# Performance work log

Measured on AMD Instinct MI355X. Metric: run time of the kernel, lower is better.

## Reference

```python
import jax, jax.numpy as jnp
import numpy as np

N, E, G = 100_000, 1_200_000, 256
EPS = 1e-5

def _bn(a, g, b):
    # BatchNorm1d in training mode: biased batch statistics over dim 0
    mu = a.mean(0)
    var = ((a - mu) ** 2).mean(0)
    return (a - mu) * jax.lax.rsqrt(var + EPS) * g + b

def _cgconv(x, src, dst, ea, Wf, bf, Ws, bs, g, b):
    # PyG CGConv: z = [x_i, x_j, edge_attr]; m = sigmoid(lin_f(z)) * softplus(lin_s(z));
    # out = BN(scatter_add(m -> dst)) + x
    z = jnp.concatenate([x[dst], x[src], ea], axis=-1)      # [E, 2*64+1]
    m = jax.nn.sigmoid(z @ Wf + bf) * jax.nn.softplus(z @ Ws + bs)  # [E, 64]
    agg = jax.ops.segment_sum(m, dst, num_segments=x.shape[0])
    return _bn(agg, g, b) + x

def setup_inputs() -> dict:
    key = jax.random.key(0)
    ks = jax.random.split(key, 16)
    def w(k, shape, scale):
        return jax.random.normal(k, shape, jnp.float32) * scale
    inp = {
        "x": jax.random.normal(ks[0], (N, 12), jnp.float32),
        "edge_index": jax.random.randint(ks[1], (2, E), 0, N, jnp.int32),
        "edge_attr": jax.random.uniform(ks[2], (E, 1), dtype=jnp.float32),
        "batch": jnp.sort(jax.random.randint(ks[3], (N,), 0, G, jnp.int32)),
        "W_in": w(ks[4], (12, 64), 0.3), "b_in": jnp.zeros((64,), jnp.float32),
        "g0": jnp.ones((64,), jnp.float32), "beta0": jnp.zeros((64,), jnp.float32),
    }
    i = 5
    for l in (1, 2, 3):
        inp[f"Wf{l}"] = w(ks[i], (129, 64), 0.1)
        inp[f"bf{l}"] = jnp.zeros((64,), jnp.float32)
        inp[f"Ws{l}"] = w(ks[i + 1], (129, 64), 0.1)
        inp[f"bs{l}"] = jnp.zeros((64,), jnp.float32)
        inp[f"g{l}"] = jnp.ones((64,), jnp.float32)
        inp[f"bb{l}"] = jnp.zeros((64,), jnp.float32)
        i += 2
    inp["W1"] = w(ks[11], (64, 32), 0.15)
    inp["b1"] = jnp.zeros((32,), jnp.float32)
    inp["W2"] = w(ks[12], (32, 1), 0.2)
    inp["b2"] = jnp.zeros((1,), jnp.float32)
    return inp

def reference(x, edge_index, edge_attr, batch,
              W_in, b_in, g0, beta0,
              Wf1, bf1, Ws1, bs1, g1, bb1,
              Wf2, bf2, Ws2, bs2, g2, bb2,
              Wf3, bf3, Ws3, bs3, g3, bb3,
              W1, b1, W2, b2):
    src, dst = edge_index[0], edge_index[1]
    h = jax.nn.relu(_bn(x @ W_in + b_in, g0, beta0))
    h = jax.nn.relu(_cgconv(h, src, dst, edge_attr, Wf1, bf1, Ws1, bs1, g1, bb1))
    h = jax.nn.relu(_cgconv(h, src, dst, edge_attr, Wf2, bf2, Ws2, bs2, g2, bb2))
    h = _cgconv(h, src, dst, edge_attr, Wf3, bf3, Ws3, bs3, g3, bb3)
    # global_mean_pool
    s = jax.ops.segment_sum(h, batch, num_segments=G)
    c = jax.ops.segment_sum(jnp.ones((h.shape[0],), h.dtype), batch, num_segments=G)
    pooled = s / jnp.maximum(c, 1.0)[:, None]
    return jax.nn.relu(pooled @ W1 + b1) @ W2 + b2  # [G, 1]
```

## Files before the change

### kernel.cpp

```cpp
#include <hip/hip_runtime.h>
#include <math.h>

#define N_NODES 100000
#define N_EDGES 1200000
#define N_GRAPHS 256
#define CH 64
#define NC (N_NODES * CH)
#define EPS 1e-5f
#define LOG2E 1.4426950408889634f
#define LN2 0.6931471805599453f
#define EA_SCALE 32768.0f

#define SCAN_NB 98
#define ZSTRN 72
#define GTILES ((N_NODES + 63) / 64)
#define EA_BLOCKS 4096
#define NW (EA_BLOCKS * 4)
#define POOL_BLOCKS 256

#define NCOLORS 8
#define SC_BLOCKS 2048
#define NCHUNK (SC_BLOCKS / NCOLORS)
#define CSZ ((N_EDGES + NCHUNK - 1) / NCHUNK)
#define RNODES ((N_NODES + NCOLORS - 1) / NCOLORS)

typedef _Float16 half8 __attribute__((ext_vector_type(8)));
typedef _Float16 half2v __attribute__((ext_vector_type(2)));
typedef float floatx4 __attribute__((ext_vector_type(4)));

__device__ __forceinline__ int lbound(const int* __restrict__ a, int n, int v) {
    int lo = 0, hi = n;
    while (lo < hi) {
        int mid = (lo + hi) >> 1;
        if (a[mid] < v) lo = mid + 1; else hi = mid;
    }
    return lo;
}

__device__ __forceinline__ float gate2(float f2, float s2) {
    float ef = __builtin_amdgcn_exp2f(-f2);
    float sig = __builtin_amdgcn_rcpf(1.0f + ef);
    float es = __builtin_amdgcn_exp2f(-fabsf(s2));
    float sp = fmaxf(s2, 0.0f) + __builtin_amdgcn_logf(1.0f + es);
    return sig * sp;
}

__global__ void embed_stats_kernel(const float* __restrict__ x,
                                   const float* __restrict__ W,
                                   const float* __restrict__ b,
                                   float* __restrict__ out,
                                   float* __restrict__ stats) {
    int c = threadIdx.x & 63;
    int sub = threadIdx.x >> 6;
    float s = 0.f, q = 0.f;
    for (int r = blockIdx.x * 4 + sub; r < N_NODES; r += gridDim.x * 4) {
        const float* xr = x + r * 12;
        float acc = b[c];
#pragma unroll
        for (int k = 0; k < 12; ++k)
            acc = fmaf(xr[k], W[k * CH + c], acc);
        out[(size_t)r * CH + c] = acc;
        s += acc;
        q = fmaf(acc, acc, q);
    }
    __shared__ float ls[4][64];
    __shared__ float lq[4][64];
    ls[sub][c] = s;
    lq[sub][c] = q;
    __syncthreads();
    if (sub == 0) {
        s = ls[0][c] + ls[1][c] + ls[2][c] + ls[3][c];
        q = lq[0][c] + lq[1][c] + lq[2][c] + lq[3][c];
        atomicAdd(&stats[c], s);
        atomicAdd(&stats[64 + c], q);
    }
}

__global__ void hist_kernel(const int* __restrict__ ei,
                            int* __restrict__ rowptr) {
    const int j = blockIdx.x & (NCOLORS - 1);
    const int k = blockIdx.x >> 3;
    const int dlo = j * RNODES;
    const int dhi = min(N_NODES, dlo + RNODES);
    const int e0 = k * CSZ;
    const int e1 = min(N_EDGES, e0 + CSZ);
    for (int e = e0 + threadIdx.x; e < e1; e += 256) {
        int d = ei[N_EDGES + e];
        if (d >= dlo && d < dhi) atomicAdd(&rowptr[d + 1], 1);
    }
}

__global__ void scanA_kernel(int* __restrict__ a, int* __restrict__ btot) {
    __shared__ int wsum[16];
    int t = threadIdx.x, lane = t & 63, w = t >> 6;
    int i = blockIdx.x * 1024 + t;
    int v = (i <= N_NODES) ? a[i] : 0;
    int s = v;
#pragma unroll
    for (int d = 1; d < 64; d <<= 1) {
        int o = __shfl_up(s, d);
        if (lane >= d) s += o;
    }
    if (lane == 63) wsum[w] = s;
    __syncthreads();
    if (w == 0) {
        int ws2 = (lane < 16) ? wsum[lane] : 0;
#pragma unroll
        for (int d = 1; d < 16; d <<= 1) {
            int o = __shfl_up(ws2, d);
            if (lane >= d) ws2 += o;
        }
        if (lane < 16) wsum[lane] = ws2;
    }
    __syncthreads();
    int off = (w > 0) ? wsum[w - 1] : 0;
    if (i <= N_NODES) a[i] = s + off;
    if (t == 0) btot[blockIdx.x] = wsum[15];
}

__global__ void scanB_kernel(int* __restrict__ btot) {
    int lane = threadIdx.x;
    int carry = 0;
    for (int base = 0; base < SCAN_NB; base += 64) {
        int i = base + lane;
        int v = (i < SCAN_NB) ? btot[i] : 0;
        int s = v;
#pragma unroll
        for (int d = 1; d < 64; d <<= 1) {
            int o = __shfl_up(s, d);
            if (lane >= d) s += o;
        }
        if (i < SCAN_NB) btot[i] = s + carry;
        carry += __shfl(s, 63);
    }
}

__global__ void scanC_kernel(int* __restrict__ a, const int* __restrict__ btot,
                             int* __restrict__ cursor) {
    int i = blockIdx.x * 1024 + threadIdx.x;
    int off = (blockIdx.x > 0) ? btot[blockIdx.x - 1] : 0;
    if (i <= N_NODES) {
        int val = a[i] + off;
        a[i] = val;
        if (i < N_NODES) cursor[i] = val;
    }
}

__global__ void scatter_kernel(const int* __restrict__ ei,
                               const float* __restrict__ ea,
                               int* __restrict__ cursor,
                               unsigned* __restrict__ sef,
                               const int* __restrict__ rowptr,
                               int* __restrict__ wrange) {
    int gid = blockIdx.x * blockDim.x + threadIdx.x;
    if (gid <= NW) {
        if (gid == NW) wrange[NW] = N_NODES;
        else {
            int e0t = (int)((long)gid * N_EDGES / NW);
            wrange[gid] = lbound(rowptr, N_NODES + 1, e0t);
        }
    }
    const int j = blockIdx.x & (NCOLORS - 1);
    const int k = blockIdx.x >> 3;
    const int dlo = j * RNODES;
    const int dhi = min(N_NODES, dlo + RNODES);
    const int e0 = k * CSZ;
    const int e1 = min(N_EDGES, e0 + CSZ);
    for (int e = e0 + threadIdx.x; e < e1; e += 256) {
        int d = ei[N_EDGES + e];
        if (d >= dlo && d < dhi) {
            int pos = atomicAdd(&cursor[d], 1);
            unsigned v = ((unsigned)ei[e] << 15) | (unsigned)(ea[e] * EA_SCALE);
            sef[pos] = v;
        }
    }
}

__global__ void prep_weights_kernel(const float* __restrict__ Wf0, const float* __restrict__ Ws0,
                                    const float* __restrict__ bf0, const float* __restrict__ bs0,
                                    const float* __restrict__ Wf1, const float* __restrict__ Ws1,
                                    const float* __restrict__ bf1, const float* __restrict__ bs1,
                                    const float* __restrict__ Wf2, const float* __restrict__ Ws2,
                                    const float* __restrict__ bf2, const float* __restrict__ bs2,
                                    _Float16* __restrict__ WT2,
                                    float* __restrict__ w128,
                                    float* __restrict__ bias) {
    int gid = blockIdx.x * blockDim.x + threadIdx.x;
    int l = gid >> 14;
    int idx = gid & 16383;
    if (l >= 3) return;
    const float* Wf = (l == 0) ? Wf0 : (l == 1) ? Wf1 : Wf2;
    const float* Ws = (l == 0) ? Ws0 : (l == 1) ? Ws1 : Ws2;
    const float* bf = (l == 0) ? bf0 : (l == 1) ? bf1 : bf2;
    const float* bs = (l == 0) ? bs0 : (l == 1) ? bs1 : bs2;
    {
        int cc = idx >> 6;
        int k = idx & 63;
        float v;
        if (cc < 128) {
            int ch = cc >> 1;
            v = (cc & 1) ? Ws[k * 64 + ch] : Wf[k * 64 + ch];
        } else {
            int j = cc - 128, ch = j >> 1;
            v = (j & 1) ? Ws[(64 + k) * 64 + ch] : Wf[(64 + k) * 64 + ch];
        }
        WT2[l * 16384 + idx] = (_Float16)(v * LOG2E);
    }
    if (idx < 128) {
        w128[l * 128 + idx] = ((idx < 64) ? Wf[128 * 64 + idx] : Ws[128 * 64 + (idx - 64)])
                              * (LOG2E / EA_SCALE);
        bias[l * 128 + idx] = ((idx < 64) ? bf[idx] : bs[idx - 64]) * LOG2E;
    }
}

template <bool RES>
__global__ __launch_bounds__(256)
void node_gemm_kernel(const float* __restrict__ ain,
                      const float* __restrict__ res,
                      const float* __restrict__ stats,
                      const float* __restrict__ gamma,
                      const float* __restrict__ beta,
                      const _Float16* __restrict__ WT2,
                      float* __restrict__ hout,
                      _Float16* __restrict__ pqrs) {
    __shared__ __align__(16) _Float16 As[64 * ZSTRN];
    __shared__ __align__(16) float ab[128];
    const int t = threadIdx.x;
    const int lane = t & 63;
    const int w = t >> 6;
    const int l15 = lane & 15;
    const int quad = lane >> 4;

    if (t < 64) {
        float mean = stats[t] * (1.0f / (float)N_NODES);
        float var  = stats[64 + t] * (1.0f / (float)N_NODES) - mean * mean;
        float inv  = rsqrtf(var + EPS);
        float A = gamma[t] * inv;
        ab[t] = A;
        ab[64 + t] = beta[t] - mean * A;
    }

    half8 bfr[4][2];
#pragma unroll
    for (int tt = 0; tt < 4; ++tt)
#pragma unroll
        for (int ks = 0; ks < 2; ++ks)
            bfr[tt][ks] = *(const half8*)(WT2 + (w * 64 + tt * 16 + l15) * 64 + ks * 32 + quad * 8);
    __syncthreads();

    const int base = blockIdx.x * 64;
    {
        const int e = t >> 2, q = t & 3;
        const int row = base + e;
        const bool valid = (row < N_NODES);
        const int crow = valid ? row : (N_NODES - 1);
        const float* ap = ain + (size_t)crow * CH + q * 16;
        const float* rp = res + (size_t)crow * CH + q * 16;
        float vv[16];
#pragma unroll
        for (int i = 0; i < 4; ++i) {
            float4 a4 = *(const float4*)(ap + i * 4);
            float4 A4 = *(const float4*)(ab + q * 16 + i * 4);
            float4 B4 = *(const float4*)(ab + 64 + q * 16 + i * 4);
            float rx = 0.f, ry = 0.f, rz = 0.f, rw = 0.f;
            if (RES) {
                float4 r4 = *(const float4*)(rp + i * 4);
                rx = r4.x; ry = r4.y; rz = r4.z; rw = r4.w;
            }
            vv[i * 4 + 0] = fmaxf(fmaf(a4.x, A4.x, B4.x) + rx, 0.0f);
            vv[i * 4 + 1] = fmaxf(fmaf(a4.y, A4.y, B4.y) + ry, 0.0f);
            vv[i * 4 + 2] = fmaxf(fmaf(a4.z, A4.z, B4.z) + rz, 0.0f);
            vv[i * 4 + 3] = fmaxf(fmaf(a4.w, A4.w, B4.w) + rw, 0.0f);
        }
        if (valid) {
            float* hp = hout + (size_t)row * CH + q * 16;
#pragma unroll
            for (int i = 0; i < 4; ++i)
                *(float4*)(hp + i * 4) = make_float4(vv[i * 4], vv[i * 4 + 1], vv[i * 4 + 2], vv[i * 4 + 3]);
        }
        half8 o;
#pragma unroll
        for (int j = 0; j < 8; ++j) o[j] = (_Float16)vv[j];
        *(half8*)(As + e * ZSTRN + q * 16) = o;
#pragma unroll
        for (int j = 0; j < 8; ++j) o[j] = (_Float16)vv[8 + j];
        *(half8*)(As + e * ZSTRN + q * 16 + 8) = o;
    }
    __syncthreads();

    floatx4 acc[4][4];
#pragma unroll
    for (int rt = 0; rt < 4; ++rt)
#pragma unroll
        for (int tt = 0; tt < 4; ++tt)
#pragma unroll
            for (int r = 0; r < 4; ++r) acc[rt][tt][r] = 0.f;

#pragma unroll
    for (int ks = 0; ks < 2; ++ks) {
#pragma unroll
        for (int rt = 0; rt < 4; ++rt) {
            half8 a = *(const half8*)(As + (rt * 16 + l15) * ZSTRN + ks * 32 + quad * 8);
#pragma unroll
            for (int tt = 0; tt < 4; ++tt)
                acc[rt][tt] = __builtin_amdgcn_mfma_f32_16x16x32_f16(a, bfr[tt][ks], acc[rt][tt], 0, 0, 0);
        }
    }

#pragma unroll
    for (int rt = 0; rt < 4; ++rt) {
#pragma unroll
        for (int r = 0; r < 4; ++r) {
            int row = base + rt * 16 + quad * 4 + r;
            if (row < N_NODES) {
#pragma unroll
                for (int tt = 0; tt < 4; ++tt)
                    pqrs[(size_t)row * 256 + w * 64 + tt * 16 + l15] = (_Float16)acc[rt][tt][r];
            }
        }
    }
}

__global__ __launch_bounds__(256)
void edge_agg_kernel(const _Float16* __restrict__ pqrs,
                     const unsigned* __restrict__ sef,
                     const int* __restrict__ rowptr,
                     const int* __restrict__ wrange,
                     const float* __restrict__ w128,
                     const float* __restrict__ bias,
                     float* __restrict__ agg,
                     float* __restrict__ wpart) {
    const int lane = threadIdx.x & 63;
    const int w = threadIdx.x >> 6;
    const int gw = __builtin_amdgcn_readfirstlane(blockIdx.x * 4 + w);
    const float wfc = w128[lane], wsc = w128[64 + lane];
    const float bfc = bias[lane], bsc = bias[64 + lane];
    const half2v* __restrict__ prb = (const half2v*)pqrs;
    const half2v* __restrict__ qsb = (const half2v*)pqrs + 64;

    const int n0 = wrange[gw];
    const int n1 = wrange[gw + 1];

    float ssum = 0.f, sqsum = 0.f;
    for (int n = n0; n < n1; ++n) {
        const int rs = rowptr[n], re = rowptr[n + 1];
        half2v pr = prb[(size_t)n * 128 + lane];
        const float fb = (float)pr[0] + bfc;
        const float sb = (float)pr[1] + bsc;
        float acc0 = 0.f, acc1 = 0.f, acc2 = 0.f, acc3 = 0.f;
        int e = rs;
        for (; e + 8 <= re; e += 8) {
            unsigned s0 = sef[e],     s1 = sef[e + 1], s2 = sef[e + 2], s3 = sef[e + 3];
            unsigned s4 = sef[e + 4], s5 = sef[e + 5], s6 = sef[e + 6], s7 = sef[e + 7];
            half2v q0 = qsb[(size_t)(s0 >> 15) * 128 + lane];
            half2v q1 = qsb[(size_t)(s1 >> 15) * 128 + lane];
            half2v q2 = qsb[(size_t)(s2 >> 15) * 128 + lane];
            half2v q3 = qsb[(size_t)(s3 >> 15) * 128 + lane];
            half2v q4 = qsb[(size_t)(s4 >> 15) * 128 + lane];
            half2v q5 = qsb[(size_t)(s5 >> 15) * 128 + lane];
            half2v q6 = qsb[(size_t)(s6 >> 15) * 128 + lane];
            half2v q7 = qsb[(size_t)(s7 >> 15) * 128 + lane];
            float ea0 = (float)(s0 & 32767u), ea1 = (float)(s1 & 32767u);
            float ea2 = (float)(s2 & 32767u), ea3 = (float)(s3 & 32767u);
            float ea4 = (float)(s4 & 32767u), ea5 = (float)(s5 & 32767u);
            float ea6 = (float)(s6 & 32767u), ea7 = (float)(s7 & 32767u);
            acc0 += gate2(fmaf(ea0, wfc, fb + (float)q0[0]), fmaf(ea0, wsc, sb + (float)q0[1]));
            acc1 += gate2(fmaf(ea1, wfc, fb + (float)q1[0]), fmaf(ea1, wsc, sb + (float)q1[1]));
            acc2 += gate2(fmaf(ea2, wfc, fb + (float)q2[0]), fmaf(ea2, wsc, sb + (float)q2[1]));
            acc3 += gate2(fmaf(ea3, wfc, fb + (float)q3[0]), fmaf(ea3, wsc, sb + (float)q3[1]));
            acc0 += gate2(fmaf(ea4, wfc, fb + (float)q4[0]), fmaf(ea4, wsc, sb + (float)q4[1]));
            acc1 += gate2(fmaf(ea5, wfc, fb + (float)q5[0]), fmaf(ea5, wsc, sb + (float)q5[1]));
            acc2 += gate2(fmaf(ea6, wfc, fb + (float)q6[0]), fmaf(ea6, wsc, sb + (float)q6[1]));
            acc3 += gate2(fmaf(ea7, wfc, fb + (float)q7[0]), fmaf(ea7, wsc, sb + (float)q7[1]));
        }
        if (e + 4 <= re) {
            unsigned s0 = sef[e], s1 = sef[e + 1], s2 = sef[e + 2], s3 = sef[e + 3];
            half2v q0 = qsb[(size_t)(s0 >> 15) * 128 + lane];
            half2v q1 = qsb[(size_t)(s1 >> 15) * 128 + lane];
            half2v q2 = qsb[(size_t)(s2 >> 15) * 128 + lane];
            half2v q3 = qsb[(size_t)(s3 >> 15) * 128 + lane];
            float ea0 = (float)(s0 & 32767u), ea1 = (float)(s1 & 32767u);
            float ea2 = (float)(s2 & 32767u), ea3 = (float)(s3 & 32767u);
            acc0 += gate2(fmaf(ea0, wfc, fb + (float)q0[0]), fmaf(ea0, wsc, sb + (float)q0[1]));
            acc1 += gate2(fmaf(ea1, wfc, fb + (float)q1[0]), fmaf(ea1, wsc, sb + (float)q1[1]));
            acc2 += gate2(fmaf(ea2, wfc, fb + (float)q2[0]), fmaf(ea2, wsc, sb + (float)q2[1]));
            acc3 += gate2(fmaf(ea3, wfc, fb + (float)q3[0]), fmaf(ea3, wsc, sb + (float)q3[1]));
            e += 4;
        }
        for (; e < re; ++e) {
            unsigned s0 = sef[e];
            half2v q0 = qsb[(size_t)(s0 >> 15) * 128 + lane];
            float ea0 = (float)(s0 & 32767u);
            acc0 += gate2(fmaf(ea0, wfc, fb + (float)q0[0]), fmaf(ea0, wsc, sb + (float)q0[1]));
        }
        float acc = LN2 * ((acc0 + acc1) + (acc2 + acc3));
        agg[(size_t)n * CH + lane] = acc;
        ssum += acc;
        sqsum = fmaf(acc, acc, sqsum);
    }
    __shared__ float reds[4][128];
    reds[w][lane] = ssum;
    reds[w][64 + lane] = sqsum;
    __syncthreads();
    if (w == 0) {
        float a = reds[0][lane] + reds[1][lane] + reds[2][lane] + reds[3][lane];
        float b = reds[0][64 + lane] + reds[1][64 + lane] + reds[2][64 + lane] + reds[3][64 + lane];
        wpart[(size_t)blockIdx.x * 128 + lane] = a;
        wpart[(size_t)blockIdx.x * 128 + 64 + lane] = b;
    }
}

__global__ __launch_bounds__(256)
void reduce_stats_kernel(const float* __restrict__ wpart,
                         float* __restrict__ stats) {
    __shared__ float red[2][128];
    const int col = threadIdx.x & 127;
    const int rg = threadIdx.x >> 7;
    const int rows = EA_BLOCKS / 128;
    const int r0 = blockIdx.x * rows;
    float s = 0.f;
    for (int r = r0 + rg; r < r0 + rows; r += 2)
        s += wpart[(size_t)r * 128 + col];
    red[rg][col] = s;
    __syncthreads();
    if (rg == 0) atomicAdd(&stats[col], red[0][col] + red[1][col]);
}

__global__ __launch_bounds__(256)
void pool_bn_kernel(const float* __restrict__ ain,
                    const float* __restrict__ res,
                    const float* __restrict__ stats,
                    const float* __restrict__ gamma,
                    const float* __restrict__ beta,
                    const int* __restrict__ batch,
                    float* __restrict__ pooled,
                    float* __restrict__ counts) {
    __shared__ float ab[128];
    if (threadIdx.x < 64) {
        int t = threadIdx.x;
        float mean = stats[t] * (1.0f / (float)N_NODES);
        float var  = stats[64 + t] * (1.0f / (float)N_NODES) - mean * mean;
        float inv  = rsqrtf(var + EPS);
        float A = gamma[t] * inv;
        ab[t] = A;
        ab[64 + t] = beta[t] - mean * A;
    }
    __syncthreads();

    const int c = threadIdx.x & 63;
    const float A = ab[c], B = ab[64 + c];
    const int walker = blockIdx.x * 4 + (threadIdx.x >> 6);
    const int nwalk = POOL_BLOCKS * 4;
    const int chunk = (N_NODES + nwalk - 1) / nwalk;
    int r0 = walker * chunk;
    int r1 = min(N_NODES, r0 + chunk);
    if (r0 >= r1) return;

    int cur = batch[r0];
    float acc = 0.0f;
    int runlen = 0;
    for (int r = r0; r < r1; ++r) {
        int b = batch[r];
        if (b != cur) {
            atomicAdd(&pooled[cur * CH + c], acc);
            if (c == 0) atomicAdd(&counts[cur], (float)runlen);
            acc = 0.0f;
            runlen = 0;
            cur = b;
        }
        size_t idx = (size_t)r * CH + c;
        acc += fmaf(ain[idx], A, B) + res[idx];
        ++runlen;
    }
    atomicAdd(&pooled[cur * CH + c], acc);
    if (c == 0) atomicAdd(&counts[cur], (float)runlen);
}

__global__ void head_kernel(const float* __restrict__ pooled,
                            const float* __restrict__ counts,
                            const float* __restrict__ W1,
                            const float* __restrict__ b1,
                            const float* __restrict__ W2,
                            const float* __restrict__ b2,
                            float* __restrict__ out) {
    int gph = blockIdx.x;
    int t = threadIdx.x;
    __shared__ float p[64];
    __shared__ float h1[32];
    float cnt = fmaxf(counts[gph], 1.0f);
    p[t] = pooled[gph * CH + t] / cnt;
    __syncthreads();
    if (t < 32) {
        float acc = b1[t];
#pragma unroll
        for (int c = 0; c < 64; ++c)
            acc = fmaf(p[c], W1[c * 32 + t], acc);
        h1[t] = fmaxf(acc, 0.0f);
    }
    __syncthreads();
    if (t == 0) {
        float acc = b2[0];
#pragma unroll
        for (int j = 0; j < 32; ++j)
            acc = fmaf(h1[j], W2[j], acc);
        out[gph] = acc;
    }
}

extern "C" void kernel_launch(void* const* d_in, const int* in_sizes, int n_in,
                              void* d_out, int out_size, void* d_ws, size_t ws_size,
                              hipStream_t stream) {
    const float* x     = (const float*)d_in[0];
    const int*   ei    = (const int*)d_in[1];
    const float* ea    = (const float*)d_in[2];
    const int*   batch = (const int*)d_in[3];
    const float* W_in  = (const float*)d_in[4];
    const float* b_in  = (const float*)d_in[5];
    const float* g0    = (const float*)d_in[6];
    const float* beta0 = (const float*)d_in[7];

    const float* Wf[3] = {(const float*)d_in[8],  (const float*)d_in[14], (const float*)d_in[20]};
    const float* bfv[3]= {(const float*)d_in[9],  (const float*)d_in[15], (const float*)d_in[21]};
    const float* Wsv[3]= {(const float*)d_in[10], (const float*)d_in[16], (const float*)d_in[22]};
    const float* bsv[3]= {(const float*)d_in[11], (const float*)d_in[17], (const float*)d_in[23]};
    const float* gm[3] = {(const float*)d_in[12], (const float*)d_in[18], (const float*)d_in[24]};
    const float* bb[3] = {(const float*)d_in[13], (const float*)d_in[19], (const float*)d_in[25]};

    const float* W1 = (const float*)d_in[26];
    const float* b1 = (const float*)d_in[27];
    const float* W2 = (const float*)d_in[28];
    const float* b2 = (const float*)d_in[29];

    float* out = (float*)d_out;

    char* base = (char*)d_ws;
    size_t off = 0;
    float* bufA = (float*)(base + off);       off += (size_t)NC * 4;
    float* bufB = (float*)(base + off);       off += (size_t)NC * 4;
    float* AGG  = (float*)(base + off);       off += (size_t)NC * 4;
    _Float16* WT2 = (_Float16*)(base + off);  off += 3 * 256 * 64 * 2;
    float* w128   = (float*)(base + off);     off += 3 * 128 * 4;
    float* biasL  = (float*)(base + off);     off += 3 * 128 * 4;
    int* cursor   = (int*)(base + off);       off += (size_t)N_NODES * 4;
    unsigned* sef = (unsigned*)(base + off);  off += (size_t)N_EDGES * 4;
    _Float16* pqrs = (_Float16*)(base + off); off += (size_t)N_NODES * 256 * 2;
    float* wpart  = (float*)(base + off);     off += (size_t)EA_BLOCKS * 128 * 4;
    int* wrange   = (int*)(base + off);       off += (size_t)(NW + 1) * 4;
    char* zbase   = base + off;
    int* rowptr   = (int*)(base + off);       off += (size_t)(N_NODES + 1) * 4;
    int* btot     = (int*)(base + off);       off += SCAN_NB * 4;
    float* stats4 = (float*)(base + off);     off += 4 * 128 * 4;
    float* pooled = (float*)(base + off);     off += (size_t)N_GRAPHS * CH * 4;
    float* counts = (float*)(base + off);     off += (size_t)N_GRAPHS * 4;
    size_t zbytes = (size_t)(base + off - zbase);

    hipMemsetAsync(zbase, 0, zbytes, stream);

    hist_kernel<<<SC_BLOCKS, 256, 0, stream>>>(ei, rowptr);
    scanA_kernel<<<SCAN_NB, 1024, 0, stream>>>(rowptr, btot);
    scanB_kernel<<<1, 64, 0, stream>>>(btot);
    scanC_kernel<<<SCAN_NB, 1024, 0, stream>>>(rowptr, btot, cursor);
    scatter_kernel<<<SC_BLOCKS, 256, 0, stream>>>(ei, ea, cursor, sef, rowptr, wrange);

    prep_weights_kernel<<<192, 256, 0, stream>>>(
        Wf[0], Wsv[0], bfv[0], bsv[0],
        Wf[1], Wsv[1], bfv[1], bsv[1],
        Wf[2], Wsv[2], bfv[2], bsv[2],
        WT2, w128, biasL);

    embed_stats_kernel<<<512, 256, 0, stream>>>(x, W_in, b_in, bufA, stats4);

    node_gemm_kernel<false><<<GTILES, 256, 0, stream>>>(
        bufA, nullptr, stats4, g0, beta0, WT2 + 0 * 256 * 64, bufB, pqrs);
    edge_agg_kernel<<<EA_BLOCKS, 256, 0, stream>>>(
        pqrs, sef, rowptr, wrange, w128 + 0 * 128, biasL + 0 * 128, AGG, wpart);
    reduce_stats_kernel<<<128, 256, 0, stream>>>(wpart, stats4 + 128);

    node_gemm_kernel<true><<<GTILES, 256, 0, stream>>>(
        AGG, bufB, stats4 + 128, gm[0], bb[0], WT2 + 1 * 256 * 64, bufA, pqrs);
    edge_agg_kernel<<<EA_BLOCKS, 256, 0, stream>>>(
        pqrs, sef, rowptr, wrange, w128 + 1 * 128, biasL + 1 * 128, AGG, wpart);
    reduce_stats_kernel<<<128, 256, 0, stream>>>(wpart, stats4 + 256);

    node_gemm_kernel<true><<<GTILES, 256, 0, stream>>>(
        AGG, bufA, stats4 + 256, gm[1], bb[1], WT2 + 2 * 256 * 64, bufB, pqrs);
    edge_agg_kernel<<<EA_BLOCKS, 256, 0, stream>>>(
        pqrs, sef, rowptr, wrange, w128 + 2 * 128, biasL + 2 * 128, AGG, wpart);
    reduce_stats_kernel<<<128, 256, 0, stream>>>(wpart, stats4 + 384);

    pool_bn_kernel<<<POOL_BLOCKS, 256, 0, stream>>>(
        AGG, bufB, stats4 + 384, gm[2], bb[2], batch, pooled, counts);
    head_kernel<<<N_GRAPHS, 64, 0, stream>>>(pooled, counts, W1, b1, W2, b2, out);
}
```

Before: 605.6 us.

## Flatten edge loop across nodes with double-buffered software-pipelined gathers

Replaces the per-node edge loop in the aggregation kernel with one flat loop over each wave's whole edge range. It issues the next 8 index loads and feature gathers into a second register set while the current 8 are consumed, and flushes node results when a row boundary is crossed. This is meant to keep more gathers in flight and avoid short-row tails and per-node loop overhead. It adds data-dependent branches per edge, more registers for the two buffers, and pads the edge array by 8 entries to cover overreads.

```diff
diff --git a/kernel.cpp b/kernel.cpp
--- a/kernel.cpp
+++ b/kernel.cpp
@@ -160,6 +160,7 @@
             wrange[gid] = lbound(rowptr, N_NODES + 1, e0t);
         }
     }
+    if (gid < 8) sef[N_EDGES + gid] = 0u;
     const int j = blockIdx.x & (NCOLORS - 1);
     const int k = blockIdx.x >> 3;
     const int dlo = j * RNODES;
@@ -321,6 +322,56 @@
     }
 }
 
+#define EA_ISSUE(p, base) \
+    r##p##0 = sef[(base) + 0]; r##p##1 = sef[(base) + 1]; \
+    r##p##2 = sef[(base) + 2]; r##p##3 = sef[(base) + 3]; \
+    r##p##4 = sef[(base) + 4]; r##p##5 = sef[(base) + 5]; \
+    r##p##6 = sef[(base) + 6]; r##p##7 = sef[(base) + 7]; \
+    q##p##0 = qsb[(size_t)(r##p##0 >> 15) * 128 + lane]; \
+    q##p##1 = qsb[(size_t)(r##p##1 >> 15) * 128 + lane]; \
+    q##p##2 = qsb[(size_t)(r##p##2 >> 15) * 128 + lane]; \
+    q##p##3 = qsb[(size_t)(r##p##3 >> 15) * 128 + lane]; \
+    q##p##4 = qsb[(size_t)(r##p##4 >> 15) * 128 + lane]; \
+    q##p##5 = qsb[(size_t)(r##p##5 >> 15) * 128 + lane]; \
+    q##p##6 = qsb[(size_t)(r##p##6 >> 15) * 128 + lane]; \
+    q##p##7 = qsb[(size_t)(r##p##7 >> 15) * 128 + lane];
+
+#define EA_FLUSH(ei_) \
+    do { \
+        float av_ = LN2 * acc; \
+        agg[(size_t)n * CH + lane] = av_; \
+        ssum += av_; sqsum = fmaf(av_, av_, sqsum); \
+        acc = 0.f; \
+        ++n; \
+        prc = prn; \
+        { int np_ = (n + 1 < N_NODES) ? (n + 1) : (N_NODES - 1); \
+          prn = prb[(size_t)np_ * 128 + lane]; } \
+        re = rowptr[n + 1]; \
+    } while (re == (ei_)); \
+    fb = (float)prc[0] + bfc; \
+    sb2 = (float)prc[1] + bsc;
+
+#define EA_EDGE(ei_, rv_, qv_) { \
+    if ((ei_) == re) { EA_FLUSH(ei_); } \
+    float eaf_ = (float)((rv_) & 32767u); \
+    float f2_ = fmaf(eaf_, wfc, fb + (float)(qv_)[0]); \
+    float s2_ = fmaf(eaf_, wsc, sb2 + (float)(qv_)[1]); \
+    acc += gate2(f2_, s2_); }
+
+#define EA_EDGE_G(ei_, rv_, qv_) if ((ei_) < E1) EA_EDGE(ei_, rv_, qv_)
+
+#define EA_CONS8(p, base) \
+    EA_EDGE((base) + 0, r##p##0, q##p##0) EA_EDGE((base) + 1, r##p##1, q##p##1) \
+    EA_EDGE((base) + 2, r##p##2, q##p##2) EA_EDGE((base) + 3, r##p##3, q##p##3) \
+    EA_EDGE((base) + 4, r##p##4, q##p##4) EA_EDGE((base) + 5, r##p##5, q##p##5) \
+    EA_EDGE((base) + 6, r##p##6, q##p##6) EA_EDGE((base) + 7, r##p##7, q##p##7)
+
+#define EA_TAIL8(p, base) \
+    EA_EDGE_G((base) + 0, r##p##0, q##p##0) EA_EDGE_G((base) + 1, r##p##1, q##p##1) \
+    EA_EDGE_G((base) + 2, r##p##2, q##p##2) EA_EDGE_G((base) + 3, r##p##3, q##p##3) \
+    EA_EDGE_G((base) + 4, r##p##4, q##p##4) EA_EDGE_G((base) + 5, r##p##5, q##p##5) \
+    EA_EDGE_G((base) + 6, r##p##6, q##p##6) EA_EDGE_G((base) + 7, r##p##7, q##p##7)
+
 __global__ __launch_bounds__(256)
 void edge_agg_kernel(const _Float16* __restrict__ pqrs,
                      const unsigned* __restrict__ sef,
@@ -342,61 +393,50 @@
     const int n1 = wrange[gw + 1];
 
     float ssum = 0.f, sqsum = 0.f;
-    for (int n = n0; n < n1; ++n) {
-        const int rs = rowptr[n], re = rowptr[n + 1];
-        half2v pr = prb[(size_t)n * 128 + lane];
-        const float fb = (float)pr[0] + bfc;
-        const float sb = (float)pr[1] + bsc;
-        float acc0 = 0.f, acc1 = 0.f, acc2 = 0.f, acc3 = 0.f;
-        int e = rs;
-        for (; e + 8 <= re; e += 8) {
-            unsigned s0 = sef[e],     s1 = sef[e + 1], s2 = sef[e + 2], s3 = sef[e + 3];
-            unsigned s4 = sef[e + 4], s5 = sef[e + 5], s6 = sef[e + 6], s7 = sef[e + 7];
-            half2v q0 = qsb[(size_t)(s0 >> 15) * 128 + lane];
-            half2v q1 = qsb[(size_t)(s1 >> 15) * 128 + lane];
-            half2v q2 = qsb[(size_t)(s2 >> 15) * 128 + lane];
-            half2v q3 = qsb[(size_t)(s3 >> 15) * 128 + lane];
-            half2v q4 = qsb[(size_t)(s4 >> 15) * 128 + lane];
-            half2v q5 = qsb[(size_t)(s5 >> 15) * 128 + lane];
-            half2v q6 = qsb[(size_t)(s6 >> 15) * 128 + lane];
-            half2v q7 = qsb[(size_t)(s7 >> 15) * 128 + lane];
-            float ea0 = (float)(s0 & 32767u), ea1 = (float)(s1 & 32767u);
-            float ea2 = (float)(s2 & 32767u), ea3 = (float)(s3 & 32767u);
-            float ea4 = (float)(s4 & 32767u), ea5 = (float)(s5 & 32767u);
-            float ea6 = (float)(s6 & 32767u), ea7 = (float)(s7 & 32767u);
-            acc0 += gate2(fmaf(ea0, wfc, fb + (float)q0[0]), fmaf(ea0, wsc, sb + (float)q0[1]));
-            acc1 += gate2(fmaf(ea1, wfc, fb + (float)q1[0]), fmaf(ea1, wsc, sb + (float)q1[1]));
-            acc2 += gate2(fmaf(ea2, wfc, fb + (float)q2[0]), fmaf(ea2, wsc, sb + (float)q2[1]));
-            acc3 += gate2(fmaf(ea3, wfc, fb + (float)q3[0]), fmaf(ea3, wsc, sb + (float)q3[1]));
-            acc0 += gate2(fmaf(ea4, wfc, fb + (float)q4[0]), fmaf(ea4, wsc, sb + (float)q4[1]));
-            acc1 += gate2(fmaf(ea5, wfc, fb + (float)q5[0]), fmaf(ea5, wsc, sb + (float)q5[1]));
-            acc2 += gate2(fmaf(ea6, wfc, fb + (float)q6[0]), fmaf(ea6, wsc, sb + (float)q6[1]));
-            acc3 += gate2(fmaf(ea7, wfc, fb + (float)q7[0]), fmaf(ea7, wsc, sb + (float)q7[1]));
-        }
-        if (e + 4 <= re) {
-            unsigned s0 = sef[e], s1 = sef[e + 1], s2 = sef[e + 2], s3 = sef[e + 3];
-            half2v q0 = qsb[(size_t)(s0 >> 15) * 128 + lane];
-            half2v q1 = qsb[(size_t)(s1 >> 15) * 128 + lane];
-            half2v q2 = qsb[(size_t)(s2 >> 15) * 128 + lane];
-            half2v q3 = qsb[(size_t)(s3 >> 15) * 128 + lane];
-            float ea0 = (float)(s0 & 32767u), ea1 = (float)(s1 & 32767u);
-            float ea2 = (float)(s2 & 32767u), ea3 = (float)(s3 & 32767u);
-            acc0 += gate2(fmaf(ea0, wfc, fb + (float)q0[0]), fmaf(ea0, wsc, sb + (float)q0[1]));
-            acc1 += gate2(fmaf(ea1, wfc, fb + (float)q1[0]), fmaf(ea1, wsc, sb + (float)q1[1]));
-            acc2 += gate2(fmaf(ea2, wfc, fb + (float)q2[0]), fmaf(ea2, wsc, sb + (float)q2[1]));
-            acc3 += gate2(fmaf(ea3, wfc, fb + (float)q3[0]), fmaf(ea3, wsc, sb + (float)q3[1]));
-            e += 4;
-        }
-        for (; e < re; ++e) {
-            unsigned s0 = sef[e];
-            half2v q0 = qsb[(size_t)(s0 >> 15) * 128 + lane];
-            float ea0 = (float)(s0 & 32767u);
-            acc0 += gate2(fmaf(ea0, wfc, fb + (float)q0[0]), fmaf(ea0, wsc, sb + (float)q0[1]));
-        }
-        float acc = LN2 * ((acc0 + acc1) + (acc2 + acc3));
-        agg[(size_t)n * CH + lane] = acc;
-        ssum += acc;
-        sqsum = fmaf(acc, acc, sqsum);
+    if (n0 < n1) {
+        int n = n0;
+        int re = rowptr[n + 1];
+        const int E1 = rowptr[n1];
+        int eb = rowptr[n0];
+
+        half2v prc = prb[(size_t)n * 128 + lane];
+        int np0 = (n + 1 < N_NODES) ? (n + 1) : (N_NODES - 1);
+        half2v prn = prb[(size_t)np0 * 128 + lane];
+        float fb = (float)prc[0] + bfc;
+        float sb2 = (float)prc[1] + bsc;
+        float acc = 0.f;
+
+        unsigned ra0, ra1, ra2, ra3, ra4, ra5, ra6, ra7;
+        unsigned rb0, rb1, rb2, rb3, rb4, rb5, rb6, rb7;
+        half2v qa0, qa1, qa2, qa3, qa4, qa5, qa6, qa7;
+        half2v qb0, qb1, qb2, qb3, qb4, qb5, qb6, qb7;
+
+        EA_ISSUE(a, eb);
+        while (eb + 8 <= E1) {
+            int ebn = eb + 8;
+            if (ebn < E1) { EA_ISSUE(b, ebn); }
+            EA_CONS8(a, eb);
+            eb = ebn;
+            if (eb + 8 > E1) {
+                EA_TAIL8(b, eb);
+                eb = E1;
+                goto edges_done;
+            }
+            ebn = eb + 8;
+            if (ebn < E1) { EA_ISSUE(a, ebn); }
+            EA_CONS8(b, eb);
+            eb = ebn;
+        }
+        EA_TAIL8(a, eb);
+edges_done:
+        while (n < n1) {
+            float av = LN2 * acc;
+            agg[(size_t)n * CH + lane] = av;
+            ssum += av;
+            sqsum = fmaf(av, av, sqsum);
+            acc = 0.f;
+            ++n;
+        }
     }
     __shared__ float reds[4][128];
     reds[w][lane] = ssum;
@@ -542,7 +582,7 @@
     float* w128   = (float*)(base + off);     off += 3 * 128 * 4;
     float* biasL  = (float*)(base + off);     off += 3 * 128 * 4;
     int* cursor   = (int*)(base + off);       off += (size_t)N_NODES * 4;
-    unsigned* sef = (unsigned*)(base + off);  off += (size_t)N_EDGES * 4;
+    unsigned* sef = (unsigned*)(base + off);  off += (size_t)(N_EDGES + 8) * 4;
     _Float16* pqrs = (_Float16*)(base + off); off += (size_t)N_NODES * 256 * 2;
     float* wpart  = (float*)(base + off);     off += (size_t)EA_BLOCKS * 128 * 4;
     int* wrange   = (int*)(base + off);       off += (size_t)(NW + 1) * 4;
```

Result: slower. 649.8 us (+7.3%).

## Fold BN-stat reduction into edge kernel atomics and consumer kernels

Applied to the files above, without the earlier changes.

Removes the separate reduce_stats kernel. Each edge_agg block now atomically adds its partial sums into one of 64 striped rows, and the following node_gemm and pool_bn kernels sum those 64 rows on entry. The number of edge_agg blocks doubles to give finer work ranges, and sef gets 8 zeroed padding entries, probably so unrolled loads past the end stay safe. This saves three launches and a global partial buffer, at the cost of float atomic contention and each consumer block redoing a small reduction.

```diff
diff --git a/kernel.cpp b/kernel.cpp
--- a/kernel.cpp
+++ b/kernel.cpp
@@ -14,9 +14,10 @@
 #define SCAN_NB 98
 #define ZSTRN 72
 #define GTILES ((N_NODES + 63) / 64)
-#define EA_BLOCKS 4096
+#define EA_BLOCKS 8192
 #define NW (EA_BLOCKS * 4)
 #define POOL_BLOCKS 256
+#define WP2ROWS 64
 
 #define NCOLORS 8
 #define SC_BLOCKS 2048
@@ -160,6 +161,7 @@
             wrange[gid] = lbound(rowptr, N_NODES + 1, e0t);
         }
     }
+    if (gid < 8) sef[N_EDGES + gid] = 0u;
     const int j = blockIdx.x & (NCOLORS - 1);
     const int k = blockIdx.x >> 3;
     const int dlo = j * RNODES;
@@ -213,7 +215,7 @@
     }
 }
 
-template <bool RES>
+template <bool RES, bool RED>
 __global__ __launch_bounds__(256)
 void node_gemm_kernel(const float* __restrict__ ain,
                       const float* __restrict__ res,
@@ -225,15 +227,27 @@
                       _Float16* __restrict__ pqrs) {
     __shared__ __align__(16) _Float16 As[64 * ZSTRN];
     __shared__ __align__(16) float ab[128];
+    __shared__ float sw[128];
     const int t = threadIdx.x;
     const int lane = t & 63;
     const int w = t >> 6;
     const int l15 = lane & 15;
     const int quad = lane >> 4;
 
+    if (RED) {
+        if (t < 128) {
+            float s = 0.f;
+#pragma unroll 8
+            for (int r = 0; r < WP2ROWS; ++r) s += stats[r * 128 + t];
+            sw[t] = s;
+        }
+        __syncthreads();
+    }
     if (t < 64) {
-        float mean = stats[t] * (1.0f / (float)N_NODES);
-        float var  = stats[64 + t] * (1.0f / (float)N_NODES) - mean * mean;
+        float s0 = RED ? sw[t] : stats[t];
+        float s1 = RED ? sw[64 + t] : stats[64 + t];
+        float mean = s0 * (1.0f / (float)N_NODES);
+        float var  = s1 * (1.0f / (float)N_NODES) - mean * mean;
         float inv  = rsqrtf(var + EPS);
         float A = gamma[t] * inv;
         ab[t] = A;
@@ -329,7 +343,7 @@
                      const float* __restrict__ w128,
                      const float* __restrict__ bias,
                      float* __restrict__ agg,
-                     float* __restrict__ wpart) {
+                     float* __restrict__ wpart2) {
     const int lane = threadIdx.x & 63;
     const int w = threadIdx.x >> 6;
     const int gw = __builtin_amdgcn_readfirstlane(blockIdx.x * 4 + w);
@@ -405,41 +419,34 @@
     if (w == 0) {
         float a = reds[0][lane] + reds[1][lane] + reds[2][lane] + reds[3][lane];
         float b = reds[0][64 + lane] + reds[1][64 + lane] + reds[2][64 + lane] + reds[3][64 + lane];
-        wpart[(size_t)blockIdx.x * 128 + lane] = a;
-        wpart[(size_t)blockIdx.x * 128 + 64 + lane] = b;
-    }
-}
-
-__global__ __launch_bounds__(256)
-void reduce_stats_kernel(const float* __restrict__ wpart,
-                         float* __restrict__ stats) {
-    __shared__ float red[2][128];
-    const int col = threadIdx.x & 127;
-    const int rg = threadIdx.x >> 7;
-    const int rows = EA_BLOCKS / 128;
-    const int r0 = blockIdx.x * rows;
-    float s = 0.f;
-    for (int r = r0 + rg; r < r0 + rows; r += 2)
-        s += wpart[(size_t)r * 128 + col];
-    red[rg][col] = s;
-    __syncthreads();
-    if (rg == 0) atomicAdd(&stats[col], red[0][col] + red[1][col]);
+        float* wp = wpart2 + (size_t)(blockIdx.x & (WP2ROWS - 1)) * 128;
+        atomicAdd(&wp[lane], a);
+        atomicAdd(&wp[64 + lane], b);
+    }
 }
 
 __global__ __launch_bounds__(256)
 void pool_bn_kernel(const float* __restrict__ ain,
                     const float* __restrict__ res,
-                    const float* __restrict__ stats,
+                    const float* __restrict__ wp2,
                     const float* __restrict__ gamma,
                     const float* __restrict__ beta,
                     const int* __restrict__ batch,
                     float* __restrict__ pooled,
                     float* __restrict__ counts) {
+    __shared__ float sw[128];
     __shared__ float ab[128];
+    if (threadIdx.x < 128) {
+        float s = 0.f;
+#pragma unroll 8
+        for (int r = 0; r < WP2ROWS; ++r) s += wp2[r * 128 + threadIdx.x];
+        sw[threadIdx.x] = s;
+    }
+    __syncthreads();
     if (threadIdx.x < 64) {
         int t = threadIdx.x;
-        float mean = stats[t] * (1.0f / (float)N_NODES);
-        float var  = stats[64 + t] * (1.0f / (float)N_NODES) - mean * mean;
+        float mean = sw[t] * (1.0f / (float)N_NODES);
+        float var  = sw[64 + t] * (1.0f / (float)N_NODES) - mean * mean;
         float inv  = rsqrtf(var + EPS);
         float A = gamma[t] * inv;
         ab[t] = A;
@@ -542,14 +549,14 @@
     float* w128   = (float*)(base + off);     off += 3 * 128 * 4;
     float* biasL  = (float*)(base + off);     off += 3 * 128 * 4;
     int* cursor   = (int*)(base + off);       off += (size_t)N_NODES * 4;
-    unsigned* sef = (unsigned*)(base + off);  off += (size_t)N_EDGES * 4;
+    unsigned* sef = (unsigned*)(base + off);  off += (size_t)(N_EDGES + 8) * 4;
     _Float16* pqrs = (_Float16*)(base + off); off += (size_t)N_NODES * 256 * 2;
-    float* wpart  = (float*)(base + off);     off += (size_t)EA_BLOCKS * 128 * 4;
     int* wrange   = (int*)(base + off);       off += (size_t)(NW + 1) * 4;
     char* zbase   = base + off;
     int* rowptr   = (int*)(base + off);       off += (size_t)(N_NODES + 1) * 4;
     int* btot     = (int*)(base + off);       off += SCAN_NB * 4;
-    float* stats4 = (float*)(base + off);     off += 4 * 128 * 4;
+    float* stats0 = (float*)(base + off);     off += 128 * 4;
+    float* wpart2 = (float*)(base + off);     off += 3 * WP2ROWS * 128 * 4;
     float* pooled = (float*)(base + off);     off += (size_t)N_GRAPHS * CH * 4;
     float* counts = (float*)(base + off);     off += (size_t)N_GRAPHS * 4;
     size_t zbytes = (size_t)(base + off - zbase);
@@ -568,27 +575,27 @@
         Wf[2], Wsv[2], bfv[2], bsv[2],
         WT2, w128, biasL);
 
-    embed_stats_kernel<<<512, 256, 0, stream>>>(x, W_in, b_in, bufA, stats4);
-
-    node_gemm_kernel<false><<<GTILES, 256, 0, stream>>>(
-        bufA, nullptr, stats4, g0, beta0, WT2 + 0 * 256 * 64, bufB, pqrs);
+    embed_stats_kernel<<<512, 256, 0, stream>>>(x, W_in, b_in, bufA, stats0);
+
+    node_gemm_kernel<false, false><<<GTILES, 256, 0, stream>>>(
+        bufA, nullptr, stats0, g0, beta0, WT2 + 0 * 256 * 64, bufB, pqrs);
     edge_agg_kernel<<<EA_BLOCKS, 256, 0, stream>>>(
-        pqrs, sef, rowptr, wrange, w128 + 0 * 128, biasL + 0 * 128, AGG, wpart);
-    reduce_stats_kernel<<<128, 256, 0, stream>>>(wpart, stats4 + 128);
-
-    node_gemm_kernel<true><<<GTILES, 256, 0, stream>>>(
-        AGG, bufB, stats4 + 128, gm[0], bb[0], WT2 + 1 * 256 * 64, bufA, pqrs);
+        pqrs, sef, rowptr, wrange, w128 + 0 * 128, biasL + 0 * 128, AGG,
+        wpart2 + 0 * WP2ROWS * 128);
+
+    node_gemm_kernel<true, true><<<GTILES, 256, 0, stream>>>(
+        AGG, bufB, wpart2 + 0 * WP2ROWS * 128, gm[0], bb[0], WT2 + 1 * 256 * 64, bufA, pqrs);
     edge_agg_kernel<<<EA_BLOCKS, 256, 0, stream>>>(
-        pqrs, sef, rowptr, wrange, w128 + 1 * 128, biasL + 1 * 128, AGG, wpart);
-    reduce_stats_kernel<<<128, 256, 0, stream>>>(wpart, stats4 + 256);
-
-    node_gemm_kernel<true><<<GTILES, 256, 0, stream>>>(
-        AGG, bufA, stats4 + 256, gm[1], bb[1], WT2 + 2 * 256 * 64, bufB, pqrs);
+        pqrs, sef, rowptr, wrange, w128 + 1 * 128, biasL + 1 * 128, AGG,
+        wpart2 + 1 * WP2ROWS * 128);
+
+    node_gemm_kernel<true, true><<<GTILES, 256, 0, stream>>>(
+        AGG, bufA, wpart2 + 1 * WP2ROWS * 128, gm[1], bb[1], WT2 + 2 * 256 * 64, bufB, pqrs);
     edge_agg_kernel<<<EA_BLOCKS, 256, 0, stream>>>(
-        pqrs, sef, rowptr, wrange, w128 + 2 * 128, biasL + 2 * 128, AGG, wpart);
-    reduce_stats_kernel<<<128, 256, 0, stream>>>(wpart, stats4 + 384);
+        pqrs, sef, rowptr, wrange, w128 + 2 * 128, biasL + 2 * 128, AGG,
+        wpart2 + 2 * WP2ROWS * 128);
 
     pool_bn_kernel<<<POOL_BLOCKS, 256, 0, stream>>>(
-        AGG, bufB, stats4 + 384, gm[2], bb[2], batch, pooled, counts);
+        AGG, bufB, wpart2 + 2 * WP2ROWS * 128, gm[2], bb[2], batch, pooled, counts);
     head_kernel<<<N_GRAPHS, 64, 0, stream>>>(pooled, counts, W1, b1, W2, b2, out);
 }
```

After: 629.9 us. +4.0%, slower.
